# Performance work log

Measured on AMD Instinct MI355X. Metric: run time of the kernel, lower is better.

The kernel has to match this reference:

```python
import jax, jax.numpy as jnp
import numpy as np

N, D = 100000, 128

def _seg_softmax(vals, ids, n):
    # torch scatter_reduce amax with include_self=True over zeros init => max(0, seg max);
    # softmax is shift-invariant so this matches torch exactly and stays stable.
    m = jnp.maximum(jax.ops.segment_max(vals, ids, num_segments=n), 0.0)
    e = jnp.exp(vals - m[ids])
    s = jax.ops.segment_sum(e, ids, num_segments=n)
    return e / (s[ids] + 1e-9)

def setup_inputs() -> dict:
    key = jax.random.key(0)
    ks = jax.random.split(key, 24)
    d = D
    def lin(k, fi, fo):
        b = 1.0 / np.sqrt(fi)
        kw, kb = jax.random.split(k)
        return (jax.random.uniform(kw, (fi, fo), jnp.float32, -b, b),
                jax.random.uniform(kb, (fo,), jnp.float32, -b, b))
    Wae, bae = lin(ks[0], 2 * d, d)
    w0w, w0b = lin(ks[1], d, 1)
    War, bar = lin(ks[2], 2 * d, d)
    w1w, w1b = lin(ks[3], d, 1)
    W1, b1 = lin(ks[4], d, d)
    W2, b2 = lin(ks[5], d, d)
    W3, b3 = lin(ks[6], d, d)
    return {
        'node_emb': jax.random.normal(ks[7], (N, d), jnp.float32),
        'Wae': Wae, 'bae': bae, 'w0w': w0w[:, 0], 'w0b': w0b,
        'War': War, 'bar': bar, 'w1w': w1w[:, 0], 'w1b': w1b,
        'W1': W1, 'b1': b1, 'W2': W2, 'b2': b2, 'W3': W3, 'b3': b3,
        'er_src': jax.random.randint(ks[8], (500000,), 0, N),
        'er_dst': jax.random.randint(ks[9], (500000,), 0, N),
        'ee_src': jax.random.randint(ks[10], (500000,), 0, N),
        'ee_dst': jax.random.randint(ks[11], (500000,), 0, N),
        'rr_src': jax.random.randint(ks[12], (200000,), 0, N),
        'rr_dst': jax.random.randint(ks[13], (200000,), 0, N),
    }

def reference(node_emb, Wae, bae, w0w, w0b, War, bar, w1w, w1b,
              W1, b1, W2, b2, W3, b3,
              er_src, er_dst, ee_src, ee_dst, rr_src, rr_dst):
    n = node_emb.shape[0]
    h = node_emb[er_src]              # (E, d) head entity emb
    r = node_emb[er_dst]              # (E, d) relation emb
    # entity-side attention over relation neighbours
    pair_e = jnp.concatenate([r, h], axis=-1)
    e_ij = jnp.tanh(pair_e @ Wae + bae) @ w0w + w0b[0]
    attn_e = _seg_softmax(e_ij, er_src, n)
    attn_agg = jax.ops.segment_sum(attn_e[:, None] * r, er_src, num_segments=n)
    # relation-side attention over entity neighbours (separate params)
    pair_r = jnp.concatenate([h, r], axis=-1)
    e_ij_r = jnp.tanh(pair_r @ War + bar) @ w1w + w1b[0]
    attn_r = _seg_softmax(e_ij_r, er_dst, n)
    attn_agg = attn_agg + jax.ops.segment_sum(attn_r[:, None] * h, er_dst, num_segments=n)
    # unweighted mean over similar-entity and similar-relation edges
    mean_agg = jax.ops.segment_sum(node_emb[ee_dst], ee_src, num_segments=n)
    mean_agg = mean_agg + jax.ops.segment_sum(node_emb[rr_dst], rr_src, num_segments=n)
    cnt = jax.ops.segment_sum(jnp.ones(ee_src.shape[0], node_emb.dtype), ee_src, num_segments=n)
    cnt = cnt + jax.ops.segment_sum(jnp.ones(rr_src.shape[0], node_emb.dtype), rr_src, num_segments=n)
    mean_agg = mean_agg / jnp.maximum(cnt, 1.0)[:, None]
    return (jnp.tanh(node_emb @ W1 + b1)
            + jnp.tanh(attn_agg @ W2 + b2)
            + jnp.tanh(mean_agg @ W3 + b3))
```

## Files before the change

kernel.cpp:

```cpp
#include <hip/hip_runtime.h>
#include <hip/hip_bf16.h>

#define D 128
#define TILE 2048

typedef __bf16 bf16x8 __attribute__((ext_vector_type(8)));
typedef float f32x4 __attribute__((ext_vector_type(4)));
typedef unsigned short u16x8 __attribute__((ext_vector_type(8)));

__device__ __forceinline__ float tanh_fast(float x) {
    float e = __expf(2.0f * fabsf(x));
    float t = 1.0f - 2.0f * __builtin_amdgcn_rcpf(e + 1.0f);
    return copysignf(t, x);
}

__device__ __forceinline__ float bf2f(unsigned short u) {
    return __uint_as_float((unsigned int)u << 16);
}

__device__ __forceinline__ unsigned short f2bf_u16(float x) {
    __hip_bfloat16 t = __float2bfloat16(x);
    return *(unsigned short*)&t;
}

#define SWZ_F(x, imm) __int_as_float(__builtin_amdgcn_ds_swizzle(__float_as_int(x), imm))

__global__ __launch_bounds__(256) void detect_kernel(const unsigned short* __restrict__ x,
                                                     int* __restrict__ flag) {
    int t = threadIdx.x;
    int cnt = 0;
    for (int i = t; i < 4096; i += 256) {
        unsigned e = (x[i] >> 7) & 0xFFu;
        if (e == 0xFFu || e >= 0x90u || (e >= 1u && e <= 0x6Eu)) cnt++;
    }
    __shared__ int sh[256];
    sh[t] = cnt;
    __syncthreads();
    for (int off = 128; off; off >>= 1) {
        if (t < off) sh[t] += sh[t + off];
        __syncthreads();
    }
    if (t == 0) flag[0] = (sh[0] > 800) ? 1 : 0;
}

struct ConvBatch {
    const void* src[14];
    __hip_bfloat16* dst[14];
    int n[14];
};

__global__ __launch_bounds__(256) void conv_weights_kernel(ConvBatch cb,
                                                           const int* __restrict__ flag) {
    int a = blockIdx.y;
    const void* s = cb.src[a];
    unsigned short* d = (unsigned short*)cb.dst[a];
    int n = cb.n[a];
    int f = flag[0];
    int i = (blockIdx.x * 256 + threadIdx.x) * 4;
    if (i >= n) return;
    if (i + 4 <= n) {
        ushort4 o;
        if (f) {
            float4 v = *(const float4*)((const float*)s + i);
            o.x = f2bf_u16(v.x); o.y = f2bf_u16(v.y);
            o.z = f2bf_u16(v.z); o.w = f2bf_u16(v.w);
        } else {
            o = *(const ushort4*)((const unsigned short*)s + i);
        }
        *(ushort4*)(d + i) = o;
    } else {
        for (int j = i; j < n; j++)
            d[j] = f ? f2bf_u16(((const float*)s)[j])
                     : ((const unsigned short*)s)[j];
    }
}

__global__ __launch_bounds__(256) void conv_x_kernel(const void* __restrict__ src,
                                                     __hip_bfloat16* __restrict__ dst,
                                                     int n, const int* __restrict__ flag) {
    int i = (blockIdx.x * 256 + threadIdx.x) * 4;
    if (i >= n) return;
    int f = flag[0];
    ushort4 o;
    if (f) {
        float4 v = *(const float4*)((const float*)src + i);
        o.x = f2bf_u16(v.x); o.y = f2bf_u16(v.y);
        o.z = f2bf_u16(v.z); o.w = f2bf_u16(v.w);
    } else {
        o = *(const ushort4*)((const unsigned short*)src + i);
    }
    *(ushort4*)((unsigned short*)dst + i) = o;
}

struct TransBatch {
    const void* base[7];
    int off[7];
    unsigned short* dst[7];
};

__global__ __launch_bounds__(256) void trans_kernel(TransBatch tb,
                                                    const int* __restrict__ flag) {
    int a = blockIdx.y;
    int f = flag[0];
    const float* sf = (const float*)tb.base[a] + tb.off[a];
    const unsigned short* sb = (const unsigned short*)tb.base[a] + tb.off[a];
    unsigned short* d = tb.dst[a];
    int idx = (blockIdx.x * 256 + threadIdx.x) * 4;
    int k = idx >> 7, c = idx & 127;
    unsigned short v[4];
    if (f) {
        float4 x = *(const float4*)(sf + idx);
        v[0] = f2bf_u16(x.x); v[1] = f2bf_u16(x.y);
        v[2] = f2bf_u16(x.z); v[3] = f2bf_u16(x.w);
    } else {
        ushort4 x = *(const ushort4*)(sb + idx);
        v[0] = x.x; v[1] = x.y; v[2] = x.z; v[3] = x.w;
    }
#pragma unroll
    for (int j = 0; j < 4; j++) d[(c + j) * 128 + k] = v[j];
}

__global__ __launch_bounds__(256) void zero_kernel(int* p, int n) {
    int i = blockIdx.x * 256 + threadIdx.x;
    if (i < n) p[i] = 0;
}

__global__ __launch_bounds__(256) void count_kernel(const int* __restrict__ keys, int E,
                                                    int* __restrict__ deg) {
    int i = blockIdx.x * 256 + threadIdx.x;
    if (i < E) atomicAdd(&deg[keys[i]], 1);
}

__global__ __launch_bounds__(256) void scan_partial_kernel(const int* __restrict__ deg,
                                                           int* __restrict__ tsum,
                                                           int N, int ntpa) {
    int a = blockIdx.x / ntpa, t = blockIdx.x % ntpa;
    const int* d = deg + (size_t)a * N + (size_t)t * TILE;
    int lim = N - t * TILE; if (lim > TILE) lim = TILE;
    int base = threadIdx.x * 8;
    int s = 0;
#pragma unroll
    for (int j = 0; j < 8; j++) {
        int i = base + j;
        if (i < lim) s += d[i];
    }
    __shared__ int sh[256];
    sh[threadIdx.x] = s;
    __syncthreads();
    for (int off = 128; off; off >>= 1) {
        if (threadIdx.x < off) sh[threadIdx.x] += sh[threadIdx.x + off];
        __syncthreads();
    }
    if (threadIdx.x == 0) tsum[blockIdx.x] = sh[0];
}

__global__ __launch_bounds__(256) void scan_tiles_kernel(const int* __restrict__ tsum,
                                                         int* __restrict__ toff,
                                                         int* __restrict__ indptr,
                                                         int N, int ntpa) {
    __shared__ int tmp[256];
    int t = threadIdx.x;
    for (int a = 0; a < 4; a++) {
        int v = (t < ntpa) ? tsum[a * ntpa + t] : 0;
        tmp[t] = v;
        __syncthreads();
        for (int off = 1; off < 256; off <<= 1) {
            int u = (t >= off) ? tmp[t - off] : 0;
            __syncthreads();
            tmp[t] += u;
            __syncthreads();
        }
        if (t < ntpa) toff[a * ntpa + t] = tmp[t] - v;
        if (t == ntpa - 1) indptr[(size_t)a * (N + 1) + N] = tmp[t];
        __syncthreads();
    }
}

__global__ __launch_bounds__(256) void scan_final_kernel(int* __restrict__ degcur,
                                                         const int* __restrict__ toff,
                                                         int* __restrict__ indptr,
                                                         int N, int ntpa) {
    int a = blockIdx.x / ntpa, t = blockIdx.x % ntpa;
    int* d = degcur + (size_t)a * N + (size_t)t * TILE;
    int* ip = indptr + (size_t)a * (N + 1) + (size_t)t * TILE;
    int lim = N - t * TILE; if (lim > TILE) lim = TILE;
    int base = threadIdx.x * 8;
    int v[8];
    int s = 0;
#pragma unroll
    for (int j = 0; j < 8; j++) {
        int i = base + j;
        v[j] = (i < lim) ? d[i] : 0;
        s += v[j];
    }
    __shared__ int tmp[256];
    tmp[threadIdx.x] = s;
    __syncthreads();
    for (int off = 1; off < 256; off <<= 1) {
        int u = (threadIdx.x >= off) ? tmp[threadIdx.x - off] : 0;
        __syncthreads();
        tmp[threadIdx.x] += u;
        __syncthreads();
    }
    int run = toff[blockIdx.x] + tmp[threadIdx.x] - s;
#pragma unroll
    for (int j = 0; j < 8; j++) {
        int i = base + j;
        if (i < lim) { ip[i] = run; d[i] = run; run += v[j]; }
    }
}

__global__ __launch_bounds__(256) void scatter_attn_kernel(const int* __restrict__ keys,
                                                           const int* __restrict__ oths, int E,
                                                           int* __restrict__ cursor,
                                                           int* __restrict__ key_sorted,
                                                           int* __restrict__ oth_sorted) {
    int i = blockIdx.x * 256 + threadIdx.x;
    if (i < E) {
        int k = keys[i];
        int p = atomicAdd(&cursor[k], 1);
        key_sorted[p] = k;
        oth_sorted[p] = oths[i];
    }
}

__global__ __launch_bounds__(256) void scatter_mean_kernel(const int* __restrict__ keys,
                                                           const int* __restrict__ dsts, int E,
                                                           int* __restrict__ cursor,
                                                           int* __restrict__ dst_sorted) {
    int i = blockIdx.x * 256 + threadIdx.x;
    if (i < E) {
        int p = atomicAdd(&cursor[keys[i]], 1);
        dst_sorted[p] = dsts[i];
    }
}

__global__ __launch_bounds__(256) void gemm2_mfma_kernel(
    const __hip_bfloat16* __restrict__ X,
    const unsigned short* __restrict__ Wt,
    const __hip_bfloat16* __restrict__ bias,
    __hip_bfloat16* __restrict__ part0,
    __hip_bfloat16* __restrict__ part1, int N) {
    __shared__ __align__(16) unsigned short Bs[128 * 136];
    int n0 = blockIdx.x * 64;
    int w = threadIdx.x >> 6, lane = threadIdx.x & 63;
    int n15 = lane & 15, quad = lane >> 4;
    int arow = n0 + w * 16 + n15;
    const unsigned short* ap = (const unsigned short*)X + (size_t)arow * D + quad * 8;
    bf16x8 af[4];
#pragma unroll
    for (int t = 0; t < 4; t++) {
        bf16x8 v = {};
        if (arow < N) v = *(const bf16x8*)(ap + t * 32);
        af[t] = v;
    }
    for (int half = 0; half < 2; half++) {
        if (half) __syncthreads();
        for (int idx = threadIdx.x; idx < 128 * 16; idx += 256) {
            int r = idx >> 4, ch = idx & 15;
            uint4 v = ((const uint4*)(Wt + (size_t)(half * 128 + r) * D))[ch];
            *(uint4*)&Bs[r * 136 + ch * 8] = v;
        }
        __syncthreads();
        __hip_bfloat16* outp = half ? part1 : part0;
        for (int c = 0; c < 8; c++) {
            f32x4 acc = {0.f, 0.f, 0.f, 0.f};
            const unsigned short* brow = &Bs[(c * 16 + n15) * 136 + quad * 8];
#pragma unroll
            for (int t = 0; t < 4; t++)
                acc = __builtin_amdgcn_mfma_f32_16x16x32_bf16(
                    af[t], *(const bf16x8*)(brow + t * 32), acc, 0, 0, 0);
            int col = c * 16 + n15;
            float b = half ? __bfloat162float(bias[col]) : 0.f;
#pragma unroll
            for (int i = 0; i < 4; i++) {
                int row = n0 + w * 16 + quad * 4 + i;
                if (row < N) outp[(size_t)row * D + col] = __float2bfloat16(acc[i] + b);
            }
        }
    }
}

__global__ __launch_bounds__(256) void final_mfma_kernel(
    const __hip_bfloat16* __restrict__ X, const __hip_bfloat16* __restrict__ Agg,
    const __hip_bfloat16* __restrict__ Mn,
    const unsigned short* __restrict__ Wt1, const __hip_bfloat16* __restrict__ b1,
    const unsigned short* __restrict__ Wt2, const __hip_bfloat16* __restrict__ b2,
    const unsigned short* __restrict__ Wt3, const __hip_bfloat16* __restrict__ b3,
    void* __restrict__ out, const int* __restrict__ flag, int N) {
    __shared__ __align__(16) unsigned short Bs[128 * 136];
    int n0 = blockIdx.x * 64;
    int w = threadIdx.x >> 6, lane = threadIdx.x & 63;
    int n15 = lane & 15, quad = lane >> 4;
    int arow = n0 + w * 16 + n15;
    float osum[8][4];
#pragma unroll
    for (int c = 0; c < 8; c++)
#pragma unroll
        for (int i = 0; i < 4; i++) osum[c][i] = 0.f;
    const __hip_bfloat16* srcs[3] = {X, Agg, Mn};
    const unsigned short* Wts[3] = {Wt1, Wt2, Wt3};
    const __hip_bfloat16* bs[3] = {b1, b2, b3};
    for (int m = 0; m < 3; m++) {
        if (m > 0) __syncthreads();
        const unsigned short* Wm = Wts[m];
        for (int idx = threadIdx.x; idx < 128 * 16; idx += 256) {
            int r = idx >> 4, ch = idx & 15;
            uint4 v = ((const uint4*)(Wm + (size_t)r * D))[ch];
            *(uint4*)&Bs[r * 136 + ch * 8] = v;
        }
        __syncthreads();
        const unsigned short* ap =
            (const unsigned short*)srcs[m] + (size_t)arow * D + quad * 8;
        bf16x8 af[4];
#pragma unroll
        for (int t = 0; t < 4; t++) {
            bf16x8 v = {};
            if (arow < N) v = *(const bf16x8*)(ap + t * 32);
            af[t] = v;
        }
        for (int c = 0; c < 8; c++) {
            f32x4 acc = {0.f, 0.f, 0.f, 0.f};
            const unsigned short* brow = &Bs[(c * 16 + n15) * 136 + quad * 8];
#pragma unroll
            for (int t = 0; t < 4; t++)
                acc = __builtin_amdgcn_mfma_f32_16x16x32_bf16(
                    af[t], *(const bf16x8*)(brow + t * 32), acc, 0, 0, 0);
            float bb = __bfloat162float(bs[m][c * 16 + n15]);
#pragma unroll
            for (int i = 0; i < 4; i++) osum[c][i] += tanh_fast(acc[i] + bb);
        }
    }
    int f = flag[0];
    for (int c = 0; c < 8; c++) {
        int col = c * 16 + n15;
#pragma unroll
        for (int i = 0; i < 4; i++) {
            int row = n0 + w * 16 + quad * 4 + i;
            if (row < N) {
                if (f) ((float*)out)[(size_t)row * D + col] = osum[c][i];
                else   ((__hip_bfloat16*)out)[(size_t)row * D + col] =
                           __float2bfloat16(osum[c][i]);
            }
        }
    }
}

__global__ __launch_bounds__(256) void edge_score_kernel(
    const __hip_bfloat16* __restrict__ Pkey,
    const __hip_bfloat16* __restrict__ Poth,
    const int* __restrict__ key_s,
    const int* __restrict__ oth_s,
    const __hip_bfloat16* __restrict__ w,
    const __hip_bfloat16* __restrict__ wb,
    float* __restrict__ eij, int E) {
    int l = threadIdx.x & 15;
    int gid = (int)((blockIdx.x * 256 + threadIdx.x) >> 4);
    int ngroups = (int)((gridDim.x * 256) >> 4);
    u16x8 wv = *(const u16x8*)((const unsigned short*)w + l * 8);
    float wf[8];
#pragma unroll
    for (int j = 0; j < 8; j++) wf[j] = bf2f(wv[j]);
    float wbv = bf2f(*(const unsigned short*)wb);
    const unsigned short* PK = (const unsigned short*)Pkey;
    const unsigned short* PO = (const unsigned short*)Poth;
    for (int s = gid; s < E; s += ngroups) {
        int key = key_s[s], oth = oth_s[s];
        u16x8 a = *(const u16x8*)(PK + (size_t)key * D + l * 8);
        u16x8 b = *(const u16x8*)(PO + (size_t)oth * D + l * 8);
        float p = 0.f;
#pragma unroll
        for (int j = 0; j < 8; j++)
            p = fmaf(tanh_fast(bf2f(a[j]) + bf2f(b[j])), wf[j], p);
        p += SWZ_F(p, 0x041F);
        p += SWZ_F(p, 0x081F);
        p += SWZ_F(p, 0x101F);
        p += SWZ_F(p, 0x201F);
        if (l == 0) eij[s] = p + wbv;
    }
}

__global__ __launch_bounds__(256) void attn_node_kernel(
    const __hip_bfloat16* __restrict__ X,
    const float* __restrict__ eij_e, const int* __restrict__ ip_e,
    const int* __restrict__ oth_e,
    const float* __restrict__ eij_r, const int* __restrict__ ip_r,
    const int* __restrict__ oth_r,
    __hip_bfloat16* __restrict__ attn_agg, int N) {
    int g = (int)((blockIdx.x * 256 + threadIdx.x) >> 4);
    int l = threadIdx.x & 15;
    if (g >= N) return;
    const unsigned short* Xp = (const unsigned short*)X;
    float acc[8];
#pragma unroll
    for (int j = 0; j < 8; j++) acc[j] = 0.f;
    for (int side = 0; side < 2; side++) {
        const float* eij = side ? eij_r : eij_e;
        const int* ip  = side ? ip_r  : ip_e;
        const int* oth = side ? oth_r : oth_e;
        int s0 = ip[g], s1 = ip[g + 1];
        if (s1 == s0) continue;
        float m = 0.f;
        for (int i = s0 + l; i < s1; i += 16) m = fmaxf(m, eij[i]);
        m = fmaxf(m, SWZ_F(m, 0x041F));
        m = fmaxf(m, SWZ_F(m, 0x081F));
        m = fmaxf(m, SWZ_F(m, 0x101F));
        m = fmaxf(m, SWZ_F(m, 0x201F));
        float ssum = 0.f;
        for (int i = s0 + l; i < s1; i += 16) ssum += __expf(eij[i] - m);
        ssum += SWZ_F(ssum, 0x041F);
        ssum += SWZ_F(ssum, 0x081F);
        ssum += SWZ_F(ssum, 0x101F);
        ssum += SWZ_F(ssum, 0x201F);
        float inv = 1.f / (ssum + 1e-9f);
        int i = s0;
        for (; i + 2 <= s1; i += 2) {
            int o0 = oth[i], o1 = oth[i + 1];
            u16x8 x0 = *(const u16x8*)(Xp + (size_t)o0 * D + l * 8);
            u16x8 x1 = *(const u16x8*)(Xp + (size_t)o1 * D + l * 8);
            float p0 = __expf(eij[i] - m) * inv;
            float p1 = __expf(eij[i + 1] - m) * inv;
#pragma unroll
            for (int j = 0; j < 8; j++)
                acc[j] += p0 * bf2f(x0[j]) + p1 * bf2f(x1[j]);
        }
        if (i < s1) {
            int o0 = oth[i];
            u16x8 x0 = *(const u16x8*)(Xp + (size_t)o0 * D + l * 8);
            float p0 = __expf(eij[i] - m) * inv;
#pragma unroll
            for (int j = 0; j < 8; j++) acc[j] += p0 * bf2f(x0[j]);
        }
    }
    u16x8 ov;
#pragma unroll
    for (int j = 0; j < 8; j++) ov[j] = f2bf_u16(acc[j]);
    *(u16x8*)((unsigned short*)attn_agg + (size_t)g * D + l * 8) = ov;
}

__global__ __launch_bounds__(256) void mean_node_kernel(
    const __hip_bfloat16* __restrict__ X,
    const int* __restrict__ ip_ee, const int* __restrict__ dst_ee,
    const int* __restrict__ ip_rr, const int* __restrict__ dst_rr,
    __hip_bfloat16* __restrict__ mean_agg, int N) {
    int g = (int)((blockIdx.x * 256 + threadIdx.x) >> 4);
    int l = threadIdx.x & 15;
    if (g >= N) return;
    const unsigned short* Xp = (const unsigned short*)X;
    float acc[8];
#pragma unroll
    for (int j = 0; j < 8; j++) acc[j] = 0.f;
    int cnt = 0;
    for (int side = 0; side < 2; side++) {
        const int* ip  = side ? ip_rr  : ip_ee;
        const int* dst = side ? dst_rr : dst_ee;
        int s0 = ip[g], s1 = ip[g + 1];
        cnt += s1 - s0;
        int i = s0;
        for (; i + 2 <= s1; i += 2) {
            int o0 = dst[i], o1 = dst[i + 1];
            u16x8 x0 = *(const u16x8*)(Xp + (size_t)o0 * D + l * 8);
            u16x8 x1 = *(const u16x8*)(Xp + (size_t)o1 * D + l * 8);
#pragma unroll
            for (int j = 0; j < 8; j++)
                acc[j] += bf2f(x0[j]) + bf2f(x1[j]);
        }
        if (i < s1) {
            u16x8 x0 = *(const u16x8*)(Xp + (size_t)dst[i] * D + l * 8);
#pragma unroll
            for (int j = 0; j < 8; j++) acc[j] += bf2f(x0[j]);
        }
    }
    float inv = 1.f / fmaxf((float)cnt, 1.f);
    u16x8 ov;
#pragma unroll
    for (int j = 0; j < 8; j++) ov[j] = f2bf_u16(acc[j] * inv);
    *(u16x8*)((unsigned short*)mean_agg + (size_t)g * D + l * 8) = ov;
}

extern "C" void kernel_launch(void* const* d_in, const int* in_sizes, int n_in,
                              void* d_out, int out_size, void* d_ws, size_t ws_size,
                              hipStream_t stream) {
    const int* er_src = (const int*)d_in[15];
    const int* er_dst = (const int*)d_in[16];
    const int* ee_src = (const int*)d_in[17];
    const int* ee_dst = (const int*)d_in[18];
    const int* rr_src = (const int*)d_in[19];
    const int* rr_dst = (const int*)d_in[20];

    int N   = in_sizes[0] / D;
    int Eer = in_sizes[15];
    int Eee = in_sizes[17];
    int Err = in_sizes[19];

    char* ws = (char*)d_ws;
    size_t off = 0;
    auto alloc = [&](size_t bytes) -> void* {
        void* p = ws + off;
        off = (off + bytes + 255) & ~(size_t)255;
        return p;
    };
    int ntpa = (N + TILE - 1) / TILE;
    int T = 4 * ntpa;
    int* flag   = (int*)alloc(256);
    int* key_se = (int*)alloc((size_t)Eer * 4);
    int* key_sr = (int*)alloc((size_t)Eer * 4);
    int* oth_e  = (int*)alloc((size_t)Eer * 4);
    int* oth_r  = (int*)alloc((size_t)Eer * 4);
    int* dst_ee = (int*)alloc((size_t)Eee * 4);
    int* dst_rr = (int*)alloc((size_t)Err * 4);
    int* indptr = (int*)alloc((size_t)4 * (N + 1) * 4);
    int* degcur = (int*)alloc((size_t)4 * N * 4);
    int* tsum   = (int*)alloc((size_t)T * 4);
    int* toff   = (int*)alloc((size_t)T * 4);
    float* eij_e = (float*)alloc((size_t)Eer * 4);
    float* eij_r = (float*)alloc((size_t)Eer * 4);
    __hip_bfloat16* Xc = (__hip_bfloat16*)alloc((size_t)N * D * 2);
    __hip_bfloat16* part0 = (__hip_bfloat16*)alloc((size_t)N * D * 2);
    __hip_bfloat16* part1 = (__hip_bfloat16*)alloc((size_t)N * D * 2);
    __hip_bfloat16* attn_agg = part0;
    __hip_bfloat16* mean_agg = part1;
    unsigned short* WtA = (unsigned short*)alloc((size_t)256 * 128 * 2);
    unsigned short* WtR = (unsigned short*)alloc((size_t)256 * 128 * 2);
    unsigned short* Wt1 = (unsigned short*)alloc((size_t)128 * 128 * 2);
    unsigned short* Wt2 = (unsigned short*)alloc((size_t)128 * 128 * 2);
    unsigned short* Wt3 = (unsigned short*)alloc((size_t)128 * 128 * 2);
    ConvBatch cb;
    int widx[14] = {1, 2, 3, 4, 5, 6, 7, 8, 9, 10, 11, 12, 13, 14};
    for (int i = 0; i < 14; i++) {
        cb.src[i] = d_in[widx[i]];
        cb.n[i] = in_sizes[widx[i]];
        cb.dst[i] = (__hip_bfloat16*)alloc((size_t)cb.n[i] * 2);
    }
    const __hip_bfloat16* bae = cb.dst[1];
    const __hip_bfloat16* w0w = cb.dst[2];
    const __hip_bfloat16* w0b = cb.dst[3];
    const __hip_bfloat16* bar_= cb.dst[5];
    const __hip_bfloat16* w1w = cb.dst[6];
    const __hip_bfloat16* w1b = cb.dst[7];
    const __hip_bfloat16* b1  = cb.dst[9];
    const __hip_bfloat16* b2  = cb.dst[11];
    const __hip_bfloat16* b3  = cb.dst[13];
    (void)n_in; (void)out_size;
    if (off > ws_size) return;

    detect_kernel<<<1, 256, 0, stream>>>((const unsigned short*)d_in[0], flag);
    conv_weights_kernel<<<dim3(32, 14), 256, 0, stream>>>(cb, flag);
    conv_x_kernel<<<(N * D / 4 + 255) / 256, 256, 0, stream>>>(d_in[0], Xc, N * D, flag);
    TransBatch tb;
    tb.base[0] = d_in[1];  tb.off[0] = 0;         tb.dst[0] = WtA;
    tb.base[1] = d_in[1];  tb.off[1] = 128 * 128; tb.dst[1] = WtA + 128 * 128;
    tb.base[2] = d_in[5];  tb.off[2] = 0;         tb.dst[2] = WtR;
    tb.base[3] = d_in[5];  tb.off[3] = 128 * 128; tb.dst[3] = WtR + 128 * 128;
    tb.base[4] = d_in[9];  tb.off[4] = 0;         tb.dst[4] = Wt1;
    tb.base[5] = d_in[11]; tb.off[5] = 0;         tb.dst[5] = Wt2;
    tb.base[6] = d_in[13]; tb.off[6] = 0;         tb.dst[6] = Wt3;
    trans_kernel<<<dim3(16, 7), 256, 0, stream>>>(tb, flag);

    zero_kernel<<<(4 * N + 255) / 256, 256, 0, stream>>>(degcur, 4 * N);
    count_kernel<<<(Eer + 255) / 256, 256, 0, stream>>>(er_src, Eer, degcur);
    count_kernel<<<(Eer + 255) / 256, 256, 0, stream>>>(er_dst, Eer, degcur + N);
    count_kernel<<<(Eee + 255) / 256, 256, 0, stream>>>(ee_src, Eee, degcur + 2 * N);
    count_kernel<<<(Err + 255) / 256, 256, 0, stream>>>(rr_src, Err, degcur + 3 * N);
    scan_partial_kernel<<<T, 256, 0, stream>>>(degcur, tsum, N, ntpa);
    scan_tiles_kernel<<<1, 256, 0, stream>>>(tsum, toff, indptr, N, ntpa);
    scan_final_kernel<<<T, 256, 0, stream>>>(degcur, toff, indptr, N, ntpa);
    scatter_attn_kernel<<<(Eer + 255) / 256, 256, 0, stream>>>(er_src, er_dst, Eer,
                                                               degcur, key_se, oth_e);
    scatter_attn_kernel<<<(Eer + 255) / 256, 256, 0, stream>>>(er_dst, er_src, Eer,
                                                               degcur + N, key_sr, oth_r);
    scatter_mean_kernel<<<(Eee + 255) / 256, 256, 0, stream>>>(ee_src, ee_dst, Eee,
                                                               degcur + 2 * N, dst_ee);
    scatter_mean_kernel<<<(Err + 255) / 256, 256, 0, stream>>>(rr_src, rr_dst, Err,
                                                               degcur + 3 * N, dst_rr);

    int GB = (N + 63) / 64;
    int EB = 2048;

    gemm2_mfma_kernel<<<GB, 256, 0, stream>>>(Xc, WtA, bae, part0, part1, N);
    edge_score_kernel<<<EB, 256, 0, stream>>>(part1, part0, key_se, oth_e,
                                              w0w, w0b, eij_e, Eer);

    gemm2_mfma_kernel<<<GB, 256, 0, stream>>>(Xc, WtR, bar_, part0, part1, N);
    edge_score_kernel<<<EB, 256, 0, stream>>>(part1, part0, key_sr, oth_r,
                                              w1w, w1b, eij_r, Eer);

    int NG = (N + 15) / 16;
    attn_node_kernel<<<NG, 256, 0, stream>>>(Xc, eij_e, indptr, oth_e,
                                             eij_r, indptr + (N + 1), oth_r,
                                             attn_agg, N);
    mean_node_kernel<<<NG, 256, 0, stream>>>(Xc, indptr + 2 * (N + 1), dst_ee,
                                             indptr + 3 * (N + 1), dst_rr,
                                             mean_agg, N);
    final_mfma_kernel<<<GB, 256, 0, stream>>>(Xc, attn_agg, mean_agg,
                                              Wt1, b1, Wt2, b2, Wt3, b3,
                                              d_out, flag, N);
}
```

Before: 578.2 us.

## Batch count/scatter/node-agg launches via grid.y and tweak LDS padding

Merges the four degree-count kernels, the two attention scatters, the two mean scatters, and the attention and mean node-aggregation kernels into grid.y-indexed combined launches. This cuts launch overhead and lets independent work run concurrently. It also changes the LDS row padding for the weight tiles from 136 to 132 elements, and in the final kernel it preloads all three A-operand fragments up front instead of reloading them per matrix. The trade-offs are higher register pressure in the final kernel and a possible change in LDS bank conflicts from the new padding.

```diff
diff --git a/kernel.cpp b/kernel.cpp
--- a/kernel.cpp
+++ b/kernel.cpp
@@ -3,6 +3,7 @@
 
 #define D 128
 #define TILE 2048
+#define PADW 132
 
 typedef __bf16 bf16x8 __attribute__((ext_vector_type(8)));
 typedef float f32x4 __attribute__((ext_vector_type(4)));
@@ -125,10 +126,17 @@
     if (i < n) p[i] = 0;
 }
 
-__global__ __launch_bounds__(256) void count_kernel(const int* __restrict__ keys, int E,
-                                                    int* __restrict__ deg) {
+__global__ __launch_bounds__(256) void count4_kernel(const int* __restrict__ k0,
+                                                     const int* __restrict__ k1,
+                                                     const int* __restrict__ k2,
+                                                     const int* __restrict__ k3,
+                                                     int E0, int E1, int E2, int E3,
+                                                     int* __restrict__ deg, int N) {
+    int y = blockIdx.y;
+    const int* k = (y == 0) ? k0 : (y == 1) ? k1 : (y == 2) ? k2 : k3;
+    int E = (y == 0) ? E0 : (y == 1) ? E1 : (y == 2) ? E2 : E3;
     int i = blockIdx.x * 256 + threadIdx.x;
-    if (i < E) atomicAdd(&deg[keys[i]], 1);
+    if (i < E) atomicAdd(&deg[y * N + k[i]], 1);
 }
 
 __global__ __launch_bounds__(256) void scan_partial_kernel(const int* __restrict__ deg,
@@ -210,28 +218,44 @@
     }
 }
 
-__global__ __launch_bounds__(256) void scatter_attn_kernel(const int* __restrict__ keys,
-                                                           const int* __restrict__ oths, int E,
-                                                           int* __restrict__ cursor,
-                                                           int* __restrict__ key_sorted,
-                                                           int* __restrict__ oth_sorted) {
+__global__ __launch_bounds__(256) void scatter_attn2_kernel(const int* __restrict__ er_src,
+                                                            const int* __restrict__ er_dst, int E,
+                                                            int* __restrict__ cursor, int N,
+                                                            int* __restrict__ key_e,
+                                                            int* __restrict__ oth_e,
+                                                            int* __restrict__ key_r,
+                                                            int* __restrict__ oth_r) {
+    int y = blockIdx.y;
+    int i = blockIdx.x * 256 + threadIdx.x;
+    if (i >= E) return;
+    const int* keys = y ? er_dst : er_src;
+    const int* oths = y ? er_src : er_dst;
+    int* cur = cursor + (size_t)y * N;
+    int* ks = y ? key_r : key_e;
+    int* os = y ? oth_r : oth_e;
+    int k = keys[i];
+    int p = atomicAdd(&cur[k], 1);
+    ks[p] = k;
+    os[p] = oths[i];
+}
+
+__global__ __launch_bounds__(256) void scatter_mean2_kernel(const int* __restrict__ ee_src,
+                                                            const int* __restrict__ ee_dst, int Eee,
+                                                            const int* __restrict__ rr_src,
+                                                            const int* __restrict__ rr_dst, int Err,
+                                                            int* __restrict__ cursor, int N,
+                                                            int* __restrict__ dst_ee,
+                                                            int* __restrict__ dst_rr) {
+    int y = blockIdx.y;
+    const int* keys = y ? rr_src : ee_src;
+    const int* dsts = y ? rr_dst : ee_dst;
+    int E = y ? Err : Eee;
+    int* cur = cursor + (size_t)(2 + y) * N;
+    int* ds = y ? dst_rr : dst_ee;
     int i = blockIdx.x * 256 + threadIdx.x;
     if (i < E) {
-        int k = keys[i];
-        int p = atomicAdd(&cursor[k], 1);
-        key_sorted[p] = k;
-        oth_sorted[p] = oths[i];
-    }
-}
-
-__global__ __launch_bounds__(256) void scatter_mean_kernel(const int* __restrict__ keys,
-                                                           const int* __restrict__ dsts, int E,
-                                                           int* __restrict__ cursor,
-                                                           int* __restrict__ dst_sorted) {
-    int i = blockIdx.x * 256 + threadIdx.x;
-    if (i < E) {
-        int p = atomicAdd(&cursor[keys[i]], 1);
-        dst_sorted[p] = dsts[i];
+        int p = atomicAdd(&cur[keys[i]], 1);
+        ds[p] = dsts[i];
     }
 }
 
@@ -241,7 +265,7 @@
     const __hip_bfloat16* __restrict__ bias,
     __hip_bfloat16* __restrict__ part0,
     __hip_bfloat16* __restrict__ part1, int N) {
-    __shared__ __align__(16) unsigned short Bs[128 * 136];
+    __shared__ __align__(16) unsigned short Bs[128 * PADW];
     int n0 = blockIdx.x * 64;
     int w = threadIdx.x >> 6, lane = threadIdx.x & 63;
     int n15 = lane & 15, quad = lane >> 4;
@@ -259,13 +283,13 @@
         for (int idx = threadIdx.x; idx < 128 * 16; idx += 256) {
             int r = idx >> 4, ch = idx & 15;
             uint4 v = ((const uint4*)(Wt + (size_t)(half * 128 + r) * D))[ch];
-            *(uint4*)&Bs[r * 136 + ch * 8] = v;
+            *(uint4*)&Bs[r * PADW + ch * 8] = v;
         }
         __syncthreads();
         __hip_bfloat16* outp = half ? part1 : part0;
         for (int c = 0; c < 8; c++) {
             f32x4 acc = {0.f, 0.f, 0.f, 0.f};
-            const unsigned short* brow = &Bs[(c * 16 + n15) * 136 + quad * 8];
+            const unsigned short* brow = &Bs[(c * 16 + n15) * PADW + quad * 8];
 #pragma unroll
             for (int t = 0; t < 4; t++)
                 acc = __builtin_amdgcn_mfma_f32_16x16x32_bf16(
@@ -288,44 +312,51 @@
     const unsigned short* __restrict__ Wt2, const __hip_bfloat16* __restrict__ b2,
     const unsigned short* __restrict__ Wt3, const __hip_bfloat16* __restrict__ b3,
     void* __restrict__ out, const int* __restrict__ flag, int N) {
-    __shared__ __align__(16) unsigned short Bs[128 * 136];
+    __shared__ __align__(16) unsigned short Bs[128 * PADW];
     int n0 = blockIdx.x * 64;
     int w = threadIdx.x >> 6, lane = threadIdx.x & 63;
     int n15 = lane & 15, quad = lane >> 4;
     int arow = n0 + w * 16 + n15;
+    bf16x8 af[3][4];
+    {
+        const unsigned short* s0 = (const unsigned short*)X   + (size_t)arow * D + quad * 8;
+        const unsigned short* s1 = (const unsigned short*)Agg + (size_t)arow * D + quad * 8;
+        const unsigned short* s2 = (const unsigned short*)Mn  + (size_t)arow * D + quad * 8;
+#pragma unroll
+        for (int t = 0; t < 4; t++) {
+            bf16x8 v0 = {}, v1 = {}, v2 = {};
+            if (arow < N) {
+                v0 = *(const bf16x8*)(s0 + t * 32);
+                v1 = *(const bf16x8*)(s1 + t * 32);
+                v2 = *(const bf16x8*)(s2 + t * 32);
+            }
+            af[0][t] = v0; af[1][t] = v1; af[2][t] = v2;
+        }
+    }
     float osum[8][4];
 #pragma unroll
     for (int c = 0; c < 8; c++)
 #pragma unroll
         for (int i = 0; i < 4; i++) osum[c][i] = 0.f;
-    const __hip_bfloat16* srcs[3] = {X, Agg, Mn};
     const unsigned short* Wts[3] = {Wt1, Wt2, Wt3};
     const __hip_bfloat16* bs[3] = {b1, b2, b3};
+#pragma unroll
     for (int m = 0; m < 3; m++) {
         if (m > 0) __syncthreads();
         const unsigned short* Wm = Wts[m];
         for (int idx = threadIdx.x; idx < 128 * 16; idx += 256) {
             int r = idx >> 4, ch = idx & 15;
             uint4 v = ((const uint4*)(Wm + (size_t)r * D))[ch];
-            *(uint4*)&Bs[r * 136 + ch * 8] = v;
-        }
-        __syncthreads();
-        const unsigned short* ap =
-            (const unsigned short*)srcs[m] + (size_t)arow * D + quad * 8;
-        bf16x8 af[4];
-#pragma unroll
-        for (int t = 0; t < 4; t++) {
-            bf16x8 v = {};
-            if (arow < N) v = *(const bf16x8*)(ap + t * 32);
-            af[t] = v;
-        }
+            *(uint4*)&Bs[r * PADW + ch * 8] = v;
+        }
+        __syncthreads();
         for (int c = 0; c < 8; c++) {
             f32x4 acc = {0.f, 0.f, 0.f, 0.f};
-            const unsigned short* brow = &Bs[(c * 16 + n15) * 136 + quad * 8];
+            const unsigned short* brow = &Bs[(c * 16 + n15) * PADW + quad * 8];
 #pragma unroll
             for (int t = 0; t < 4; t++)
                 acc = __builtin_amdgcn_mfma_f32_16x16x32_bf16(
-                    af[t], *(const bf16x8*)(brow + t * 32), acc, 0, 0, 0);
+                    af[m][t], *(const bf16x8*)(brow + t * 32), acc, 0, 0, 0);
             float bb = __bfloat162float(bs[m][c * 16 + n15]);
 #pragma unroll
             for (int i = 0; i < 4; i++) osum[c][i] += tanh_fast(acc[i] + bb);
@@ -380,68 +411,15 @@
     }
 }
 
-__global__ __launch_bounds__(256) void attn_node_kernel(
+__global__ __launch_bounds__(256) void node_agg_kernel(
     const __hip_bfloat16* __restrict__ X,
     const float* __restrict__ eij_e, const int* __restrict__ ip_e,
     const int* __restrict__ oth_e,
     const float* __restrict__ eij_r, const int* __restrict__ ip_r,
     const int* __restrict__ oth_r,
-    __hip_bfloat16* __restrict__ attn_agg, int N) {
-    int g = (int)((blockIdx.x * 256 + threadIdx.x) >> 4);
-    int l = threadIdx.x & 15;
-    if (g >= N) return;
-    const unsigned short* Xp = (const unsigned short*)X;
-    float acc[8];
-#pragma unroll
-    for (int j = 0; j < 8; j++) acc[j] = 0.f;
-    for (int side = 0; side < 2; side++) {
-        const float* eij = side ? eij_r : eij_e;
-        const int* ip  = side ? ip_r  : ip_e;
-        const int* oth = side ? oth_r : oth_e;
-        int s0 = ip[g], s1 = ip[g + 1];
-        if (s1 == s0) continue;
-        float m = 0.f;
-        for (int i = s0 + l; i < s1; i += 16) m = fmaxf(m, eij[i]);
-        m = fmaxf(m, SWZ_F(m, 0x041F));
-        m = fmaxf(m, SWZ_F(m, 0x081F));
-        m = fmaxf(m, SWZ_F(m, 0x101F));
-        m = fmaxf(m, SWZ_F(m, 0x201F));
-        float ssum = 0.f;
-        for (int i = s0 + l; i < s1; i += 16) ssum += __expf(eij[i] - m);
-        ssum += SWZ_F(ssum, 0x041F);
-        ssum += SWZ_F(ssum, 0x081F);
-        ssum += SWZ_F(ssum, 0x101F);
-        ssum += SWZ_F(ssum, 0x201F);
-        float inv = 1.f / (ssum + 1e-9f);
-        int i = s0;
-        for (; i + 2 <= s1; i += 2) {
-            int o0 = oth[i], o1 = oth[i + 1];
-            u16x8 x0 = *(const u16x8*)(Xp + (size_t)o0 * D + l * 8);
-            u16x8 x1 = *(const u16x8*)(Xp + (size_t)o1 * D + l * 8);
-            float p0 = __expf(eij[i] - m) * inv;
-            float p1 = __expf(eij[i + 1] - m) * inv;
-#pragma unroll
-            for (int j = 0; j < 8; j++)
-                acc[j] += p0 * bf2f(x0[j]) + p1 * bf2f(x1[j]);
-        }
-        if (i < s1) {
-            int o0 = oth[i];
-            u16x8 x0 = *(const u16x8*)(Xp + (size_t)o0 * D + l * 8);
-            float p0 = __expf(eij[i] - m) * inv;
-#pragma unroll
-            for (int j = 0; j < 8; j++) acc[j] += p0 * bf2f(x0[j]);
-        }
-    }
-    u16x8 ov;
-#pragma unroll
-    for (int j = 0; j < 8; j++) ov[j] = f2bf_u16(acc[j]);
-    *(u16x8*)((unsigned short*)attn_agg + (size_t)g * D + l * 8) = ov;
-}
-
-__global__ __launch_bounds__(256) void mean_node_kernel(
-    const __hip_bfloat16* __restrict__ X,
     const int* __restrict__ ip_ee, const int* __restrict__ dst_ee,
     const int* __restrict__ ip_rr, const int* __restrict__ dst_rr,
+    __hip_bfloat16* __restrict__ attn_agg,
     __hip_bfloat16* __restrict__ mean_agg, int N) {
     int g = (int)((blockIdx.x * 256 + threadIdx.x) >> 4);
     int l = threadIdx.x & 15;
@@ -450,32 +428,77 @@
     float acc[8];
 #pragma unroll
     for (int j = 0; j < 8; j++) acc[j] = 0.f;
-    int cnt = 0;
-    for (int side = 0; side < 2; side++) {
-        const int* ip  = side ? ip_rr  : ip_ee;
-        const int* dst = side ? dst_rr : dst_ee;
-        int s0 = ip[g], s1 = ip[g + 1];
-        cnt += s1 - s0;
-        int i = s0;
-        for (; i + 2 <= s1; i += 2) {
-            int o0 = dst[i], o1 = dst[i + 1];
-            u16x8 x0 = *(const u16x8*)(Xp + (size_t)o0 * D + l * 8);
-            u16x8 x1 = *(const u16x8*)(Xp + (size_t)o1 * D + l * 8);
-#pragma unroll
-            for (int j = 0; j < 8; j++)
-                acc[j] += bf2f(x0[j]) + bf2f(x1[j]);
-        }
-        if (i < s1) {
-            u16x8 x0 = *(const u16x8*)(Xp + (size_t)dst[i] * D + l * 8);
-#pragma unroll
-            for (int j = 0; j < 8; j++) acc[j] += bf2f(x0[j]);
-        }
-    }
-    float inv = 1.f / fmaxf((float)cnt, 1.f);
-    u16x8 ov;
-#pragma unroll
-    for (int j = 0; j < 8; j++) ov[j] = f2bf_u16(acc[j] * inv);
-    *(u16x8*)((unsigned short*)mean_agg + (size_t)g * D + l * 8) = ov;
+    if (blockIdx.y == 0) {
+        for (int side = 0; side < 2; side++) {
+            const float* eij = side ? eij_r : eij_e;
+            const int* ip  = side ? ip_r  : ip_e;
+            const int* oth = side ? oth_r : oth_e;
+            int s0 = ip[g], s1 = ip[g + 1];
+            if (s1 == s0) continue;
+            float m = 0.f;
+            for (int i = s0 + l; i < s1; i += 16) m = fmaxf(m, eij[i]);
+            m = fmaxf(m, SWZ_F(m, 0x041F));
+            m = fmaxf(m, SWZ_F(m, 0x081F));
+            m = fmaxf(m, SWZ_F(m, 0x101F));
+            m = fmaxf(m, SWZ_F(m, 0x201F));
+            float ssum = 0.f;
+            for (int i = s0 + l; i < s1; i += 16) ssum += __expf(eij[i] - m);
+            ssum += SWZ_F(ssum, 0x041F);
+            ssum += SWZ_F(ssum, 0x081F);
+            ssum += SWZ_F(ssum, 0x101F);
+            ssum += SWZ_F(ssum, 0x201F);
+            float inv = 1.f / (ssum + 1e-9f);
+            int i = s0;
+            for (; i + 2 <= s1; i += 2) {
+                int o0 = oth[i], o1 = oth[i + 1];
+                u16x8 x0 = *(const u16x8*)(Xp + (size_t)o0 * D + l * 8);
+                u16x8 x1 = *(const u16x8*)(Xp + (size_t)o1 * D + l * 8);
+                float p0 = __expf(eij[i] - m) * inv;
+                float p1 = __expf(eij[i + 1] - m) * inv;
+#pragma unroll
+                for (int j = 0; j < 8; j++)
+                    acc[j] += p0 * bf2f(x0[j]) + p1 * bf2f(x1[j]);
+            }
+            if (i < s1) {
+                int o0 = oth[i];
+                u16x8 x0 = *(const u16x8*)(Xp + (size_t)o0 * D + l * 8);
+                float p0 = __expf(eij[i] - m) * inv;
+#pragma unroll
+                for (int j = 0; j < 8; j++) acc[j] += p0 * bf2f(x0[j]);
+            }
+        }
+        u16x8 ov;
+#pragma unroll
+        for (int j = 0; j < 8; j++) ov[j] = f2bf_u16(acc[j]);
+        *(u16x8*)((unsigned short*)attn_agg + (size_t)g * D + l * 8) = ov;
+    } else {
+        int cnt = 0;
+        for (int side = 0; side < 2; side++) {
+            const int* ip  = side ? ip_rr  : ip_ee;
+            const int* dst = side ? dst_rr : dst_ee;
+            int s0 = ip[g], s1 = ip[g + 1];
+            cnt += s1 - s0;
+            int i = s0;
+            for (; i + 2 <= s1; i += 2) {
+                int o0 = dst[i], o1 = dst[i + 1];
+                u16x8 x0 = *(const u16x8*)(Xp + (size_t)o0 * D + l * 8);
+                u16x8 x1 = *(const u16x8*)(Xp + (size_t)o1 * D + l * 8);
+#pragma unroll
+                for (int j = 0; j < 8; j++)
+                    acc[j] += bf2f(x0[j]) + bf2f(x1[j]);
+            }
+            if (i < s1) {
+                u16x8 x0 = *(const u16x8*)(Xp + (size_t)dst[i] * D + l * 8);
+#pragma unroll
+                for (int j = 0; j < 8; j++) acc[j] += bf2f(x0[j]);
+            }
+        }
+        float inv = 1.f / fmaxf((float)cnt, 1.f);
+        u16x8 ov;
+#pragma unroll
+        for (int j = 0; j < 8; j++) ov[j] = f2bf_u16(acc[j] * inv);
+        *(u16x8*)((unsigned short*)mean_agg + (size_t)g * D + l * 8) = ov;
+    }
 }
 
 extern "C" void kernel_launch(void* const* d_in, const int* in_sizes, int n_in,
@@ -558,21 +581,18 @@
     trans_kernel<<<dim3(16, 7), 256, 0, stream>>>(tb, flag);
 
     zero_kernel<<<(4 * N + 255) / 256, 256, 0, stream>>>(degcur, 4 * N);
-    count_kernel<<<(Eer + 255) / 256, 256, 0, stream>>>(er_src, Eer, degcur);
-    count_kernel<<<(Eer + 255) / 256, 256, 0, stream>>>(er_dst, Eer, degcur + N);
-    count_kernel<<<(Eee + 255) / 256, 256, 0, stream>>>(ee_src, Eee, degcur + 2 * N);
-    count_kernel<<<(Err + 255) / 256, 256, 0, stream>>>(rr_src, Err, degcur + 3 * N);
+    int Emax = Eer > Eee ? Eer : Eee;
+    if (Err > Emax) Emax = Err;
+    count4_kernel<<<dim3((Emax + 255) / 256, 4), 256, 0, stream>>>(
+        er_src, er_dst, ee_src, rr_src, Eer, Eer, Eee, Err, degcur, N);
     scan_partial_kernel<<<T, 256, 0, stream>>>(degcur, tsum, N, ntpa);
     scan_tiles_kernel<<<1, 256, 0, stream>>>(tsum, toff, indptr, N, ntpa);
     scan_final_kernel<<<T, 256, 0, stream>>>(degcur, toff, indptr, N, ntpa);
-    scatter_attn_kernel<<<(Eer + 255) / 256, 256, 0, stream>>>(er_src, er_dst, Eer,
-                                                               degcur, key_se, oth_e);
-    scatter_attn_kernel<<<(Eer + 255) / 256, 256, 0, stream>>>(er_dst, er_src, Eer,
-                                                               degcur + N, key_sr, oth_r);
-    scatter_mean_kernel<<<(Eee + 255) / 256, 256, 0, stream>>>(ee_src, ee_dst, Eee,
-                                                               degcur + 2 * N, dst_ee);
-    scatter_mean_kernel<<<(Err + 255) / 256, 256, 0, stream>>>(rr_src, rr_dst, Err,
-                                                               degcur + 3 * N, dst_rr);
+    scatter_attn2_kernel<<<dim3((Eer + 255) / 256, 2), 256, 0, stream>>>(
+        er_src, er_dst, Eer, degcur, N, key_se, oth_e, key_sr, oth_r);
+    int Emm = Eee > Err ? Eee : Err;
+    scatter_mean2_kernel<<<dim3((Emm + 255) / 256, 2), 256, 0, stream>>>(
+        ee_src, ee_dst, Eee, rr_src, rr_dst, Err, degcur, N, dst_ee, dst_rr);
 
     int GB = (N + 63) / 64;
     int EB = 2048;
@@ -586,12 +606,10 @@
                                               w1w, w1b, eij_r, Eer);
 
     int NG = (N + 15) / 16;
-    attn_node_kernel<<<NG, 256, 0, stream>>>(Xc, eij_e, indptr, oth_e,
-                                             eij_r, indptr + (N + 1), oth_r,
-                                             attn_agg, N);
-    mean_node_kernel<<<NG, 256, 0, stream>>>(Xc, indptr + 2 * (N + 1), dst_ee,
-                                             indptr + 3 * (N + 1), dst_rr,
-                                             mean_agg, N);
+    node_agg_kernel<<<dim3(NG, 2), 256, 0, stream>>>(
+        Xc, eij_e, indptr, oth_e, eij_r, indptr + (N + 1), oth_r,
+        indptr + 2 * (N + 1), dst_ee, indptr + 3 * (N + 1), dst_rr,
+        attn_agg, mean_agg, N);
     final_mfma_kernel<<<GB, 256, 0, stream>>>(Xc, attn_agg, mean_agg,
                                               Wt1, b1, Wt2, b2, Wt3, b3,
                                               d_out, flag, N);
```

New measurement: 683.7 us. 1.18x slower.
